# Kernel optimization log

Measured on AMD Instinct MI355X. Metric: run time of the kernel, lower is better.

Reference implementation:

```python
import jax, jax.numpy as jnp
import numpy as np

B, T, D = 2, 2048, 2048
H, HD = 16, 128            # num_heads, head_dim = D // H
DVH = 2                    # dynamic_value_num_heads
NVK = 4                    # num_v_keys = int(sqrt(H))
TOPK = DVH * 2             # = 4 <= NVK


def setup_inputs() -> dict:
    key = jax.random.key(0)
    ks = jax.random.split(key, 12)
    s = jnp.float32(0.02)
    return {
        "x": jax.random.normal(ks[0], (B, T, D), jnp.float32),
        "Wq": jax.random.normal(ks[1], (D, D), jnp.float32) * s,
        "bq": jnp.zeros((D,), jnp.float32),
        "Wk": jax.random.normal(ks[2], (D, D), jnp.float32) * s,
        "bk": jnp.zeros((D,), jnp.float32),
        "Wvq": jax.random.normal(ks[3], (HD * DVH, D), jnp.float32) * s,
        "bvq": jnp.zeros((HD * DVH,), jnp.float32),
        "v_keys": jax.random.normal(ks[4], (DVH, NVK, HD), jnp.float32) * s,
        "v_embed": jax.random.normal(ks[5], (H, HD * H), jnp.float32) * s,
        "Wo": jax.random.normal(ks[6], (D, D), jnp.float32) * s,
        "bo": jnp.zeros((D,), jnp.float32),
    }


def reference(x, Wq, bq, Wk, bk, Wvq, bvq, v_keys, v_embed, Wo, bo):
    b, t, d = x.shape
    # q/k projections -> [b, H, t, HD]
    q = (x @ Wq.T + bq).reshape(b, t, H, HD).transpose(0, 2, 1, 3)
    k = (x @ Wk.T + bk).reshape(b, t, H, HD).transpose(0, 2, 1, 3)

    # --- compute_value_states ---
    vq = (x @ Wvq.T + bvq).reshape(b, t, DVH, HD)          # [b,t,h,n]
    sim = jnp.einsum('bthn,hkn->bthk', vq, v_keys)         # [b,t,DVH,NVK]
    _, idx = jax.lax.top_k(sim, TOPK)                      # [b,t,DVH,TOPK]
    ve = v_embed[idx]                                      # gather -> [b,t,DVH,TOPK,d]
    # einsum 'btd,bthkd->btd' == x * sum over (h,k)
    vs = x * ve.sum(axis=(2, 3))                           # [b,t,d]
    v = vs.reshape(b, t, H, HD).transpose(0, 2, 1, 3)      # [b,H,t,HD]

    # --- hand-rolled causal attention ---
    scores = jnp.einsum('bhqd,bhkd->bhqk', q, k) / np.float32(np.sqrt(HD))
    min_val = jnp.finfo(x.dtype).min
    mask = jnp.triu(jnp.full((t, t), min_val, dtype=x.dtype), 1)
    scores = scores + mask
    w = jax.nn.softmax(scores.astype(jnp.float32), axis=-1).astype(x.dtype)
    o = jnp.einsum('bhqk,bhkd->bhqd', w, v)                # [b,H,t,HD]
    o = o.transpose(0, 2, 1, 3).reshape(b, t, d)
    return o @ Wo.T + bo
```

## Files before the change

### kernel.cpp

```cpp
#include <hip/hip_runtime.h>
#include <hip/hip_bf16.h>

#define DEV __device__ __forceinline__

typedef __bf16 bf16x8 __attribute__((ext_vector_type(8)));
typedef __bf16 bf16x4 __attribute__((ext_vector_type(4)));
typedef float f32x4 __attribute__((ext_vector_type(4)));

static constexpr int kB = 2, kT = 2048, kD = 2048, kH = 16, kHD = 128;
static constexpr int kBT = kB * kT;

#if __has_builtin(__builtin_amdgcn_exp2f)
DEV float fast_exp2(float x) { return __builtin_amdgcn_exp2f(x); }
#else
DEV float fast_exp2(float x) { return exp2f(x); }
#endif

DEV unsigned short f2bf(float f) {
  union { __hip_bfloat16 h; unsigned short u; } cv;
  cv.h = __float2bfloat16(f);
  return cv.u;
}

DEV void gl_lds16(const void* g, void* l) {
  __builtin_amdgcn_global_load_lds(
      (const __attribute__((address_space(1))) unsigned int*)g,
      (__attribute__((address_space(3))) unsigned int*)l, 16, 0, 0);
}

#define MFMA(a, b, c) __builtin_amdgcn_mfma_f32_16x16x32_bf16(a, b, c, 0, 0, 0)

__global__ __launch_bounds__(256) void cvt_kernel(const float* __restrict__ src,
                                                  unsigned short* __restrict__ dst,
                                                  int n4) {
  int i = blockIdx.x * 256 + threadIdx.x;
  if (i >= n4) return;
  float4 v = ((const float4*)src)[i];
  ushort4 o;
  o.x = f2bf(v.x); o.y = f2bf(v.y); o.z = f2bf(v.z); o.w = f2bf(v.w);
  ((ushort4*)dst)[i] = o;
}

__global__ __launch_bounds__(256) void cvt3_kernel(
    const float* __restrict__ s0, const float* __restrict__ s1,
    const float* __restrict__ s2, unsigned short* __restrict__ d0,
    unsigned short* __restrict__ d1, unsigned short* __restrict__ d2, int n4) {
  const float* s = blockIdx.y == 0 ? s0 : blockIdx.y == 1 ? s1 : s2;
  unsigned short* d = blockIdx.y == 0 ? d0 : blockIdx.y == 1 ? d1 : d2;
  int i = blockIdx.x * 256 + threadIdx.x;
  if (i >= n4) return;
  float4 v = ((const float4*)s)[i];
  ushort4 o;
  o.x = f2bf(v.x); o.y = f2bf(v.y); o.z = f2bf(v.z); o.w = f2bf(v.w);
  ((ushort4*)d)[i] = o;
}

__global__ __launch_bounds__(256) void make_vt_kernel(
    const float* __restrict__ x, const float* __restrict__ v_embed,
    unsigned short* __restrict__ vt) {
  const int t = blockIdx.x * 64 + (threadIdx.x & 63);
  const int h = blockIdx.y, b = blockIdx.z;
  for (int hd = (threadIdx.x >> 6); hd < kHD; hd += 4) {
    const int d = h * kHD + hd;
    const float c = 2.f * (v_embed[d] + v_embed[kD + d] + v_embed[2 * kD + d] +
                           v_embed[3 * kD + d]);
    const float v = x[(size_t)(b * kT + t) * kD + d] * c;
    vt[((size_t)((b * kH + h) * kHD + hd)) * kT + t] = f2bf(v);
  }
}

template <bool BF16OUT, bool FUSED2>
__global__ __launch_bounds__(256, 3) void gemm_bt(
    const unsigned short* __restrict__ A, const unsigned short* __restrict__ B1,
    const unsigned short* __restrict__ B2, const float* __restrict__ bias1,
    const float* __restrict__ bias2, void* __restrict__ C1, void* __restrict__ C2,
    float scale1, float scale2) {
  constexpr int N = kD, K = kD;
  __shared__ __align__(16) unsigned short As[128 * 32], Bs[128 * 32];
  const unsigned short* Bm = (FUSED2 && blockIdx.z) ? B2 : B1;
  const float* bias = (FUSED2 && blockIdx.z) ? bias2 : bias1;
  void* Cout = (FUSED2 && blockIdx.z) ? C2 : C1;
  const float scale = (FUSED2 && blockIdx.z) ? scale2 : scale1;
  const int tid = threadIdx.x;
  const int lane = tid & 63, wave = tid >> 6;
  const int wr = wave >> 1, wc = wave & 1;
  const int m0 = blockIdx.y * 128, n0 = blockIdx.x * 128;
  const int frow = lane & 15, fc = lane >> 4;

  f32x4 acc[4][4];
  for (int i = 0; i < 4; i++)
    for (int j = 0; j < 4; j++)
      for (int r = 0; r < 4; r++) acc[i][j][r] = 0.f;

  const int r0 = tid >> 2, c0 = (tid & 3) ^ (r0 & 3);
  const int p1 = tid + 256;
  const int r1 = p1 >> 2, c1 = (p1 & 3) ^ (r1 & 3);

  const unsigned short* Ab = A + (size_t)m0 * K;
  const unsigned short* Bb = Bm + (size_t)n0 * K;

  for (int k0 = 0; k0 < K; k0 += 32) {
    __syncthreads();
    gl_lds16(Ab + (size_t)r0 * K + k0 + c0 * 8, As + tid * 8);
    gl_lds16(Ab + (size_t)r1 * K + k0 + c1 * 8, As + p1 * 8);
    gl_lds16(Bb + (size_t)r0 * K + k0 + c0 * 8, Bs + tid * 8);
    gl_lds16(Bb + (size_t)r1 * K + k0 + c1 * 8, Bs + p1 * 8);
    __syncthreads();
    bf16x8 af[4], bfr[4];
    for (int mi = 0; mi < 4; mi++) {
      int row = wr * 64 + mi * 16 + frow;
      af[mi] = *(const bf16x8*)(As + (row * 4 + (fc ^ (row & 3))) * 8);
    }
    for (int ni = 0; ni < 4; ni++) {
      int row = wc * 64 + ni * 16 + frow;
      bfr[ni] = *(const bf16x8*)(Bs + (row * 4 + (fc ^ (row & 3))) * 8);
    }
    for (int mi = 0; mi < 4; mi++)
      for (int ni = 0; ni < 4; ni++)
        acc[mi][ni] = MFMA(af[mi], bfr[ni], acc[mi][ni]);
  }
  for (int ni = 0; ni < 4; ni++) {
    const int n = n0 + wc * 64 + ni * 16 + frow;
    const float bs = bias[n];
    for (int mi = 0; mi < 4; mi++) {
      const int mb = m0 + wr * 64 + mi * 16 + fc * 4;
      for (int r = 0; r < 4; r++) {
        const float v = (acc[mi][ni][r] + bs) * scale;
        if (BF16OUT)
          ((unsigned short*)Cout)[(size_t)(mb + r) * N + n] = f2bf(v);
        else
          ((float*)Cout)[(size_t)(mb + r) * N + n] = v;
      }
    }
  }
}

__global__ __launch_bounds__(256, 2) void attn2_kernel(
    const unsigned short* __restrict__ Q, const unsigned short* __restrict__ Kg,
    const unsigned short* __restrict__ Vt, unsigned short* __restrict__ O) {
  __shared__ __align__(16) unsigned short sK[2][64 * 128];
  __shared__ __align__(16) unsigned short sV[2][64 * 128];
  const int tid = threadIdx.x, l = tid & 63, w = tid >> 6;
  const int g = l >> 4, q15 = l & 15;
  const int pi = blockIdx.x, h = blockIdx.y, b = blockIdx.z;

  for (int half = 0; half < 2; half++) {
    const int qt = half == 0 ? (31 - pi) : pi;
    const int q0 = qt * 64;
    const int nkb = qt + 1;
    const int q = q0 + w * 16 + q15;

    __syncthreads();
    for (int i = 0; i < 4; i++) {
      const int idx = tid + i * 256;
      const int key = idx >> 4, cc = (idx & 15) ^ (key & 15);
      gl_lds16(Kg + (size_t)(b * kT + key) * kD + h * kHD + cc * 8,
               &sK[0][idx * 8]);
    }
    for (int i = 0; i < 4; i++) {
      const int idx = tid + i * 256;
      const int hd = idx >> 3, cc = (idx & 7) ^ (hd & 7);
      gl_lds16(Vt + ((size_t)((b * kH + h) * kHD + hd)) * kT + cc * 8,
               &sV[0][idx * 8]);
    }

    bf16x8 qf[4];
    const unsigned short* Qrow = Q + (size_t)(b * kT + q) * kD + h * kHD;
#pragma unroll
    for (int kk = 0; kk < 4; kk++)
      qf[kk] = *(const bf16x8*)(Qrow + kk * 32 + g * 8);

    f32x4 oacc[8];
#pragma unroll
    for (int ni = 0; ni < 8; ni++)
      for (int r = 0; r < 4; r++) oacc[ni][r] = 0.f;
    float m_i = -1e30f, l_i = 0.f;

    for (int kb = 0; kb < nkb; kb++) {
      const int bb = kb & 1;
      __syncthreads();
      if (kb + 1 < nkb) {
        const int k0n = (kb + 1) * 64;
        const int nb = 1 - bb;
#pragma unroll
        for (int i = 0; i < 4; i++) {
          const int idx = tid + i * 256;
          const int key = idx >> 4, cc = (idx & 15) ^ (key & 15);
          gl_lds16(Kg + (size_t)(b * kT + k0n + key) * kD + h * kHD + cc * 8,
                   &sK[nb][idx * 8]);
        }
#pragma unroll
        for (int i = 0; i < 4; i++) {
          const int idx = tid + i * 256;
          const int hd = idx >> 3, cc = (idx & 7) ^ (hd & 7);
          gl_lds16(Vt + ((size_t)((b * kH + h) * kHD + hd)) * kT + k0n + cc * 8,
                   &sV[nb][idx * 8]);
        }
      }

      f32x4 st[4];
#pragma unroll
      for (int s = 0; s < 4; s++)
        for (int r = 0; r < 4; r++) st[s][r] = 0.f;
#pragma unroll
      for (int s = 0; s < 4; s++) {
        const int key = s * 16 + q15;
#pragma unroll
        for (int kk = 0; kk < 4; kk++) {
          bf16x8 kf = *(const bf16x8*)(
              &sK[bb][(key * 16 + ((kk * 4 + g) ^ (key & 15))) * 8]);
          st[s] = MFMA(kf, qf[kk], st[s]);
        }
      }
      if (kb == nkb - 1) {
        const int k0 = kb * 64;
#pragma unroll
        for (int s = 0; s < 4; s++)
          for (int r = 0; r < 4; r++)
            if (k0 + s * 16 + g * 4 + r > q) st[s][r] = -1e30f;
      }
      float mx = -1e30f;
#pragma unroll
      for (int s = 0; s < 4; s++)
        for (int r = 0; r < 4; r++) mx = fmaxf(mx, st[s][r]);
      mx = fmaxf(mx, __shfl_xor(mx, 16, 64));
      mx = fmaxf(mx, __shfl_xor(mx, 32, 64));
      const float mn = fmaxf(m_i, mx);
      const float alpha = fast_exp2(m_i - mn);
      float rs = 0.f;
      union { bf16x8 v; unsigned short u[8]; } pkv[2];
#pragma unroll
      for (int s = 0; s < 4; s++)
        for (int r = 0; r < 4; r++) {
          const float p = fast_exp2(st[s][r] - mn);
          rs += p;
          pkv[s >> 1].u[(s & 1) * 4 + r] = f2bf(p);
        }
      rs += __shfl_xor(rs, 16, 64);
      rs += __shfl_xor(rs, 32, 64);
      m_i = mn;
      l_i = l_i * alpha + rs;
#pragma unroll
      for (int ni = 0; ni < 8; ni++)
        for (int r = 0; r < 4; r++) oacc[ni][r] *= alpha;
#pragma unroll
      for (int ni = 0; ni < 8; ni++) {
        const int hd = ni * 16 + q15;
        const int hx = hd & 7, base = hd * 8;
#pragma unroll
        for (int c = 0; c < 2; c++) {
          const int c4l = 8 * c + g;
          const int c4h = 8 * c + 4 + g;
          bf16x4 lo = *(const bf16x4*)(
              &sV[bb][(base + ((c4l >> 1) ^ hx)) * 8 + (c4l & 1) * 4]);
          bf16x4 hi = *(const bf16x4*)(
              &sV[bb][(base + ((c4h >> 1) ^ hx)) * 8 + (c4h & 1) * 4]);
          bf16x8 vf = __builtin_shufflevector(lo, hi, 0, 1, 2, 3, 4, 5, 6, 7);
          oacc[ni] = MFMA(vf, pkv[c].v, oacc[ni]);
        }
      }
    }
    const float inv = 1.f / l_i;
    unsigned short* Orow = O + (size_t)(b * kT + q) * kD + h * kHD;
#pragma unroll
    for (int ni = 0; ni < 8; ni++) {
      ushort4 o4;
      o4.x = f2bf(oacc[ni][0] * inv);
      o4.y = f2bf(oacc[ni][1] * inv);
      o4.z = f2bf(oacc[ni][2] * inv);
      o4.w = f2bf(oacc[ni][3] * inv);
      *(ushort4*)(Orow + ni * 16 + g * 4) = o4;
    }
  }
}

extern "C" void kernel_launch(void* const* d_in, const int* in_sizes, int n_in,
                              void* d_out, int out_size, void* d_ws, size_t ws_size,
                              hipStream_t stream) {
  const float* x       = (const float*)d_in[0];
  const float* Wq      = (const float*)d_in[1];
  const float* bq      = (const float*)d_in[2];
  const float* Wk      = (const float*)d_in[3];
  const float* bk      = (const float*)d_in[4];
  const float* v_embed = (const float*)d_in[8];
  const float* Wo      = (const float*)d_in[9];
  const float* bo      = (const float*)d_in[10];
  float* out = (float*)d_out;

  char* w = (char*)d_ws;
  unsigned short* xb  = (unsigned short*)w; w += (size_t)kBT * kD * 2;
  unsigned short* qb  = (unsigned short*)w; w += (size_t)kBT * kD * 2;
  unsigned short* kb  = (unsigned short*)w; w += (size_t)kBT * kD * 2;
  unsigned short* ob  = (unsigned short*)w; w += (size_t)kBT * kD * 2;
  unsigned short* vtb = (unsigned short*)w; w += (size_t)kBT * kD * 2;
  unsigned short* wqb = (unsigned short*)w; w += (size_t)kD * kD * 2;
  unsigned short* wkb = (unsigned short*)w; w += (size_t)kD * kD * 2;
  unsigned short* wob = (unsigned short*)w; w += (size_t)kD * kD * 2;

  cvt_kernel<<<kBT * kD / 1024, 256, 0, stream>>>(x, xb, kBT * kD / 4);
  cvt3_kernel<<<dim3(kD * kD / 1024, 3), 256, 0, stream>>>(
      Wq, Wk, Wo, wqb, wkb, wob, kD * kD / 4);
  make_vt_kernel<<<dim3(kT / 64, kH, kB), 256, 0, stream>>>(x, v_embed, vtb);

  const float scaleQ = 0.08838834764831845f * 1.4426950408889634f;
  gemm_bt<true, true><<<dim3(kD / 128, kBT / 128, 2), 256, 0, stream>>>(
      xb, wqb, wkb, bq, bk, qb, kb, scaleQ, 1.0f);

  attn2_kernel<<<dim3(16, kH, kB), 256, 0, stream>>>(qb, kb, vtb, ob);

  gemm_bt<false, false><<<dim3(kD / 128, kBT / 128, 1), 256, 0, stream>>>(
      ob, wob, nullptr, bo, nullptr, out, nullptr, 1.0f, 1.0f);
}
```

Baseline: 368.5 us.

## Retune swizzles, tile-transpose value build, remap attention blocks, merge conversion launches

```diff
diff --git a/kernel.cpp b/kernel.cpp
--- a/kernel.cpp
+++ b/kernel.cpp
@@ -30,23 +30,18 @@
 
 #define MFMA(a, b, c) __builtin_amdgcn_mfma_f32_16x16x32_bf16(a, b, c, 0, 0, 0)
 
-__global__ __launch_bounds__(256) void cvt_kernel(const float* __restrict__ src,
-                                                  unsigned short* __restrict__ dst,
-                                                  int n4) {
-  int i = blockIdx.x * 256 + threadIdx.x;
-  if (i >= n4) return;
-  float4 v = ((const float4*)src)[i];
-  ushort4 o;
-  o.x = f2bf(v.x); o.y = f2bf(v.y); o.z = f2bf(v.z); o.w = f2bf(v.w);
-  ((ushort4*)dst)[i] = o;
-}
-
-__global__ __launch_bounds__(256) void cvt3_kernel(
+DEV int swz4(int row) { return (row ^ (row >> 2)) & 3; }
+
+__global__ __launch_bounds__(256) void cvt4_kernel(
     const float* __restrict__ s0, const float* __restrict__ s1,
-    const float* __restrict__ s2, unsigned short* __restrict__ d0,
-    unsigned short* __restrict__ d1, unsigned short* __restrict__ d2, int n4) {
-  const float* s = blockIdx.y == 0 ? s0 : blockIdx.y == 1 ? s1 : s2;
-  unsigned short* d = blockIdx.y == 0 ? d0 : blockIdx.y == 1 ? d1 : d2;
+    const float* __restrict__ s2, const float* __restrict__ s3,
+    unsigned short* __restrict__ d0, unsigned short* __restrict__ d1,
+    unsigned short* __restrict__ d2, unsigned short* __restrict__ d3,
+    int n0, int n1) {
+  const int y = blockIdx.y;
+  const float* s = y == 0 ? s0 : y == 1 ? s1 : y == 2 ? s2 : s3;
+  unsigned short* d = y == 0 ? d0 : y == 1 ? d1 : y == 2 ? d2 : d3;
+  const int n4 = y == 0 ? n0 : n1;
   int i = blockIdx.x * 256 + threadIdx.x;
   if (i >= n4) return;
   float4 v = ((const float4*)s)[i];
@@ -58,19 +53,41 @@
 __global__ __launch_bounds__(256) void make_vt_kernel(
     const float* __restrict__ x, const float* __restrict__ v_embed,
     unsigned short* __restrict__ vt) {
-  const int t = blockIdx.x * 64 + (threadIdx.x & 63);
-  const int h = blockIdx.y, b = blockIdx.z;
-  for (int hd = (threadIdx.x >> 6); hd < kHD; hd += 4) {
-    const int d = h * kHD + hd;
-    const float c = 2.f * (v_embed[d] + v_embed[kD + d] + v_embed[2 * kD + d] +
-                           v_embed[3 * kD + d]);
-    const float v = x[(size_t)(b * kT + t) * kD + d] * c;
-    vt[((size_t)((b * kH + h) * kHD + hd)) * kT + t] = f2bf(v);
+  __shared__ __align__(16) unsigned short sT[128 * 72];
+  const int t0 = blockIdx.x * 64, h = blockIdx.y, b = blockIdx.z;
+  const int tid = threadIdx.x;
+  const int d4 = tid & 31, r8 = tid >> 5;
+  const int dg = h * kHD + d4 * 4;
+  float4 e0 = *(const float4*)(v_embed + dg);
+  float4 e1 = *(const float4*)(v_embed + kD + dg);
+  float4 e2 = *(const float4*)(v_embed + 2 * kD + dg);
+  float4 e3 = *(const float4*)(v_embed + 3 * kD + dg);
+  float4 c4;
+  c4.x = 2.f * (e0.x + e1.x + e2.x + e3.x);
+  c4.y = 2.f * (e0.y + e1.y + e2.y + e3.y);
+  c4.z = 2.f * (e0.z + e1.z + e2.z + e3.z);
+  c4.w = 2.f * (e0.w + e1.w + e2.w + e3.w);
+#pragma unroll
+  for (int it = 0; it < 8; it++) {
+    const int t = r8 + it * 8;
+    float4 v = *(const float4*)(x + (size_t)(b * kT + t0 + t) * kD + dg);
+    sT[(d4 * 4 + 0) * 72 + t] = f2bf(v.x * c4.x);
+    sT[(d4 * 4 + 1) * 72 + t] = f2bf(v.y * c4.y);
+    sT[(d4 * 4 + 2) * 72 + t] = f2bf(v.z * c4.z);
+    sT[(d4 * 4 + 3) * 72 + t] = f2bf(v.w * c4.w);
+  }
+  __syncthreads();
+#pragma unroll
+  for (int it = 0; it < 4; it++) {
+    const int hd = (tid >> 3) + it * 32;
+    const int tt = (tid & 7) * 8;
+    bf16x8 vv = *(const bf16x8*)(sT + hd * 72 + tt);
+    *(bf16x8*)(vt + ((size_t)((b * kH + h) * kHD + hd)) * kT + t0 + tt) = vv;
   }
 }
 
 template <bool BF16OUT, bool FUSED2>
-__global__ __launch_bounds__(256, 3) void gemm_bt(
+__global__ __launch_bounds__(256, 4) void gemm_bt(
     const unsigned short* __restrict__ A, const unsigned short* __restrict__ B1,
     const unsigned short* __restrict__ B2, const float* __restrict__ bias1,
     const float* __restrict__ bias2, void* __restrict__ C1, void* __restrict__ C2,
@@ -92,9 +109,9 @@
     for (int j = 0; j < 4; j++)
       for (int r = 0; r < 4; r++) acc[i][j][r] = 0.f;
 
-  const int r0 = tid >> 2, c0 = (tid & 3) ^ (r0 & 3);
+  const int r0 = tid >> 2, c0 = (tid & 3) ^ swz4(r0);
   const int p1 = tid + 256;
-  const int r1 = p1 >> 2, c1 = (p1 & 3) ^ (r1 & 3);
+  const int r1 = p1 >> 2, c1 = (p1 & 3) ^ swz4(r1);
 
   const unsigned short* Ab = A + (size_t)m0 * K;
   const unsigned short* Bb = Bm + (size_t)n0 * K;
@@ -109,11 +126,11 @@
     bf16x8 af[4], bfr[4];
     for (int mi = 0; mi < 4; mi++) {
       int row = wr * 64 + mi * 16 + frow;
-      af[mi] = *(const bf16x8*)(As + (row * 4 + (fc ^ (row & 3))) * 8);
+      af[mi] = *(const bf16x8*)(As + (row * 4 + (fc ^ swz4(row))) * 8);
     }
     for (int ni = 0; ni < 4; ni++) {
       int row = wc * 64 + ni * 16 + frow;
-      bfr[ni] = *(const bf16x8*)(Bs + (row * 4 + (fc ^ (row & 3))) * 8);
+      bfr[ni] = *(const bf16x8*)(Bs + (row * 4 + (fc ^ swz4(row))) * 8);
     }
     for (int mi = 0; mi < 4; mi++)
       for (int ni = 0; ni < 4; ni++)
@@ -142,7 +159,11 @@
   __shared__ __align__(16) unsigned short sV[2][64 * 128];
   const int tid = threadIdx.x, l = tid & 63, w = tid >> 6;
   const int g = l >> 4, q15 = l & 15;
-  const int pi = blockIdx.x, h = blockIdx.y, b = blockIdx.z;
+  const int bid = blockIdx.x;
+  const int xcd = bid & 7, rest = bid >> 3;
+  const int gidx = xcd + 8 * (rest & 3);
+  const int pi = rest >> 2;
+  const int h = gidx & 15, b = gidx >> 4;
 
   for (int half = 0; half < 2; half++) {
     const int qt = half == 0 ? (31 - pi) : pi;
@@ -159,7 +180,8 @@
     }
     for (int i = 0; i < 4; i++) {
       const int idx = tid + i * 256;
-      const int hd = idx >> 3, cc = (idx & 7) ^ (hd & 7);
+      const int hd = idx >> 3;
+      const int cc = (idx & 7) ^ (hd & 7) ^ (((hd >> 3) & 1) << 2);
       gl_lds16(Vt + ((size_t)((b * kH + h) * kHD + hd)) * kT + cc * 8,
                &sV[0][idx * 8]);
     }
@@ -192,7 +214,8 @@
 #pragma unroll
         for (int i = 0; i < 4; i++) {
           const int idx = tid + i * 256;
-          const int hd = idx >> 3, cc = (idx & 7) ^ (hd & 7);
+          const int hd = idx >> 3;
+          const int cc = (idx & 7) ^ (hd & 7) ^ (((hd >> 3) & 1) << 2);
           gl_lds16(Vt + ((size_t)((b * kH + h) * kHD + hd)) * kT + k0n + cc * 8,
                    &sV[nb][idx * 8]);
         }
@@ -246,7 +269,7 @@
 #pragma unroll
       for (int ni = 0; ni < 8; ni++) {
         const int hd = ni * 16 + q15;
-        const int hx = hd & 7, base = hd * 8;
+        const int hx = (hd & 7) ^ (((hd >> 3) & 1) << 2), base = hd * 8;
 #pragma unroll
         for (int c = 0; c < 2; c++) {
           const int c4l = 8 * c + g;
@@ -297,16 +320,15 @@
   unsigned short* wkb = (unsigned short*)w; w += (size_t)kD * kD * 2;
   unsigned short* wob = (unsigned short*)w; w += (size_t)kD * kD * 2;
 
-  cvt_kernel<<<kBT * kD / 1024, 256, 0, stream>>>(x, xb, kBT * kD / 4);
-  cvt3_kernel<<<dim3(kD * kD / 1024, 3), 256, 0, stream>>>(
-      Wq, Wk, Wo, wqb, wkb, wob, kD * kD / 4);
+  cvt4_kernel<<<dim3(kBT * kD / 1024, 4), 256, 0, stream>>>(
+      x, Wq, Wk, Wo, xb, wqb, wkb, wob, kBT * kD / 4, kD * kD / 4);
   make_vt_kernel<<<dim3(kT / 64, kH, kB), 256, 0, stream>>>(x, v_embed, vtb);
 
   const float scaleQ = 0.08838834764831845f * 1.4426950408889634f;
   gemm_bt<true, true><<<dim3(kD / 128, kBT / 128, 2), 256, 0, stream>>>(
       xb, wqb, wkb, bq, bk, qb, kb, scaleQ, 1.0f);
 
-  attn2_kernel<<<dim3(16, kH, kB), 256, 0, stream>>>(qb, kb, vtb, ob);
+  attn2_kernel<<<dim3(512), 256, 0, stream>>>(qb, kb, vtb, ob);
 
   gemm_bt<false, false><<<dim3(kD / 128, kBT / 128, 1), 256, 0, stream>>>(
       ob, wob, nullptr, bo, nullptr, out, nullptr, 1.0f, 1.0f);
```

Result: faster. 337.6 us (-8.4%).
